# Kernel tuning notes

Hardware: AMD Instinct MI355X
Metric: run time of the kernel (lower is better)

Reference implementation:

```python
import jax, jax.numpy as jnp
import numpy as np
import math

N_HEADS = 12
ROPE_DIM = 64
BASE = 10000.0


def _rope_tables(seq_len, dim):
    inv_freq = 1.0 / (BASE ** (jnp.arange(0, dim, 2, dtype=jnp.float32) / dim))
    t = jnp.arange(seq_len, dtype=jnp.float32)
    freqs = jnp.outer(t, inv_freq)                      # [S, dim/2]
    emb = jnp.concatenate([freqs, freqs], axis=-1)      # [S, dim]
    # broadcast shape [1, S, 1, dim]
    return jnp.cos(emb)[None, :, None, :], jnp.sin(emb)[None, :, None, :]


def _rotate_half(x):
    x1, x2 = jnp.split(x, 2, axis=-1)
    return jnp.concatenate([-x2, x1], axis=-1)


def setup_inputs() -> dict:
    key = jax.random.key(0)
    ks = jax.random.split(key, 9)
    B, S, E = 2, 2048, 768
    s = 1.0 / math.sqrt(E)
    return {
        "x": jax.random.normal(ks[0], (B, S, E), jnp.float32),
        "Wq": jax.random.normal(ks[1], (E, E), jnp.float32) * s,
        "bq": jax.random.normal(ks[2], (E,), jnp.float32) * 0.02,
        "Wk": jax.random.normal(ks[3], (E, E), jnp.float32) * s,
        "bk": jax.random.normal(ks[4], (E,), jnp.float32) * 0.02,
        "Wv": jax.random.normal(ks[5], (E, E), jnp.float32) * s,
        "bv": jax.random.normal(ks[6], (E,), jnp.float32) * 0.02,
        "Wp": jax.random.normal(ks[7], (E, E), jnp.float32) * s,
        "bp": jax.random.normal(ks[8], (E,), jnp.float32) * 0.02,
    }


def reference(x, Wq, bq, Wk, bk, Wv, bv, Wp, bp):
    B, S, E = x.shape
    H = N_HEADS
    D = E // H

    q = (x @ Wq + bq).reshape(B, S, H, D)
    k = (x @ Wk + bk).reshape(B, S, H, D)
    v = (x @ Wv + bv).reshape(B, S, H, D)

    # rotary on first ROPE_DIM dims (here ROPE_DIM == D, so full rotary)
    cos, sin = _rope_tables(S, ROPE_DIM)
    q_rot, q_pass = q[..., :ROPE_DIM], q[..., ROPE_DIM:]
    k_rot, k_pass = k[..., :ROPE_DIM], k[..., ROPE_DIM:]
    q_rot = q_rot * cos + _rotate_half(q_rot) * sin
    k_rot = k_rot * cos + _rotate_half(k_rot) * sin
    q = jnp.concatenate([q_rot, q_pass], axis=-1)
    k = jnp.concatenate([k_rot, k_pass], axis=-1)

    # scores [B, M, N, H]; mask before scaling (as in the torch code; -inf unchanged)
    att = jnp.einsum("bmhd,bnhd->bmnh", q, k)
    causal = jnp.tril(jnp.ones((S, S), dtype=bool))[None, :, :, None]
    att = jnp.where(causal, att, -jnp.inf)
    att = jax.nn.softmax(att / math.sqrt(D), axis=2)
    out = jnp.einsum("bmnh,bnhd->bmhd", att, v)

    return out.reshape(B, S, E) @ Wp + bp
```

## Files before the change

### kernel.cpp

```cpp
#include <hip/hip_runtime.h>
#include <stdint.h>

#define S_LEN 2048
#define EMB   768
#define NH    12
#define DH    64
#define M_TOT 4096
#define WELEM 589824
#define QELEM 3145728

typedef float  floatx4 __attribute__((ext_vector_type(4)));
typedef __bf16 bf16x8  __attribute__((ext_vector_type(8)));
typedef __bf16 bf16x4  __attribute__((ext_vector_type(4)));
typedef unsigned short ushortx4 __attribute__((ext_vector_type(4)));

__device__ __forceinline__ unsigned short f2bf(float f) {
    union { float f; unsigned u; } v; v.f = f;
    unsigned u = v.u;
    unsigned r = (u + 0x7FFFu + ((u >> 16) & 1u)) >> 16;
    return (unsigned short)r;
}

__device__ __forceinline__ void gl_lds16(const void* g, void* l) {
    __builtin_amdgcn_global_load_lds(
        (__attribute__((address_space(1))) const void*)g,
        (__attribute__((address_space(3))) void*)l, 16, 0, 0);
}

__global__ void cvt_all_kernel(const float* __restrict__ x, unsigned short* __restrict__ xb,
                               const float* __restrict__ W0, const float* __restrict__ W1,
                               const float* __restrict__ W2, const float* __restrict__ W3,
                               unsigned short* __restrict__ WT_all, float2* __restrict__ rope) {
    __shared__ float t[64][65];
    const int blk = blockIdx.x;
    if (blk < 3072) {
        int i = (blk * 256 + threadIdx.x) * 4;
        float4 v = *(const float4*)(x + i);
        ushortx4 r = { f2bf(v.x), f2bf(v.y), f2bf(v.z), f2bf(v.w) };
        *(ushortx4*)(xb + i) = r;
        return;
    }
    if (blk >= 3648) {
        int idx = (blk - 3648) * 256 + threadIdx.x;
        int s = idx >> 5, d = idx & 31;
        float f = exp2f((float)d * -0.41524101186092034f);
        float th = (float)s * f;
        float sn, cs; sincosf(th, &sn, &cs);
        rope[idx] = make_float2(cs, sn);
        return;
    }
    const int tc = blk - 3072;
    const int z = tc / 144, rr0 = tc % 144;
    const float* W = (z == 0) ? W0 : (z == 1 ? W1 : (z == 2 ? W2 : W3));
    unsigned short* O = WT_all + (size_t)z * WELEM;
    const int k0 = (rr0 % 12) * 64, n0 = (rr0 / 12) * 64;
    const int c = threadIdx.x & 63, r4 = threadIdx.x >> 6;
#pragma unroll
    for (int rr = 0; rr < 64; rr += 4) {
        int r = rr + r4;
        t[r][c] = W[(size_t)(k0 + r) * EMB + n0 + c];
    }
    __syncthreads();
#pragma unroll
    for (int rr = 0; rr < 64; rr += 4) {
        int nn = rr + r4;
        O[(size_t)(n0 + nn) * EMB + k0 + c] = f2bf(t[c][nn]);
    }
}

static __device__ __forceinline__ void gemm_core_128x128(
    const unsigned short* __restrict__ A, const unsigned short* __restrict__ BT,
    int m0, int n0, int K, int tid, floatx4 (&acc)[4][4],
    unsigned short* Als, unsigned short* Bls)
{
    const int lane = tid & 63;
    const int c0 = lane & 15, quad = lane >> 4;
    const int wave = tid >> 6;
    const int wm = (wave >> 1) * 64, wn = (wave & 1) * 64;

    for (int k0 = 0; k0 < K; k0 += 64) {
        __syncthreads();
#pragma unroll
        for (int it = 0; it < 4; ++it) {
            int ch = it * 256 + tid;
            int row = ch >> 3, sc = ch & 7;
            int cc = sc ^ (row & 7);
            gl_lds16(A  + (size_t)(m0 + row) * K + k0 + cc * 8, Als + ch * 8);
            gl_lds16(BT + (size_t)(n0 + row) * K + k0 + cc * 8, Bls + ch * 8);
        }
        __syncthreads();
        bf16x8 af[4][2], bfv[4][2];
#pragma unroll
        for (int ii = 0; ii < 4; ++ii) {
            int row = wm + 16 * ii + c0;
#pragma unroll
            for (int h = 0; h < 2; ++h)
                af[ii][h] = *(const bf16x8*)(Als + row * 64 + (((4 * h + quad) ^ (row & 7)) * 8));
        }
#pragma unroll
        for (int jj = 0; jj < 4; ++jj) {
            int row = wn + 16 * jj + c0;
#pragma unroll
            for (int h = 0; h < 2; ++h)
                bfv[jj][h] = *(const bf16x8*)(Bls + row * 64 + (((4 * h + quad) ^ (row & 7)) * 8));
        }
#pragma unroll
        for (int ii = 0; ii < 4; ++ii)
#pragma unroll
            for (int jj = 0; jj < 4; ++jj) {
                acc[ii][jj] = __builtin_amdgcn_mfma_f32_16x16x32_bf16(af[ii][0], bfv[jj][0], acc[ii][jj], 0, 0, 0);
                acc[ii][jj] = __builtin_amdgcn_mfma_f32_16x16x32_bf16(af[ii][1], bfv[jj][1], acc[ii][jj], 0, 0, 0);
            }
    }
}

__global__ __launch_bounds__(256, 3) void qkv_kernel(
    const unsigned short* __restrict__ xb, const unsigned short* __restrict__ WT_all,
    const float* __restrict__ bq, const float* __restrict__ bk, const float* __restrict__ bv,
    const float2* __restrict__ rope, unsigned short* __restrict__ qkv_out)
{
    __shared__ __align__(16) unsigned short Als[128 * 64];
    __shared__ __align__(16) unsigned short Bls[128 * 64];
    const int z = blockIdx.z;
    const float* bias = (z == 0) ? bq : (z == 1 ? bk : bv);
    __bf16* Cout = (__bf16*)(qkv_out + (size_t)z * QELEM);
    const int m0 = blockIdx.x * 128, n0 = blockIdx.y * 128;
    const int tid = threadIdx.x, lane = tid & 63, c0 = lane & 15, quad = lane >> 4, wave = tid >> 6;
    const int wm = (wave >> 1) * 64, wn = (wave & 1) * 64;

    floatx4 acc[4][4] = {};
    gemm_core_128x128(xb, WT_all + (size_t)z * WELEM, m0, n0, EMB, tid, acc, Als, Bls);

    if (z == 2) {
#pragma unroll
        for (int ii = 0; ii < 4; ++ii) {
            int m = m0 + wm + 16 * ii + quad * 4;
            int b = m >> 11, s = m & (S_LEN - 1);
#pragma unroll
            for (int jj = 0; jj < 4; ++jj) {
                int n = n0 + wn + 16 * jj + c0;
                int h = n >> 6, d = n & 63;
                float bn = bias[n];
                bf16x4 pv;
#pragma unroll
                for (int r = 0; r < 4; ++r) pv[r] = (__bf16)(acc[ii][jj][r] + bn);
                *(bf16x4*)(Cout + ((size_t)(b * NH + h) * DH + d) * S_LEN + s) = pv;
            }
        }
        return;
    }

#pragma unroll
    for (int ii = 0; ii < 4; ++ii) {
#pragma unroll
        for (int r = 0; r < 4; ++r) {
            int m = m0 + wm + 16 * ii + quad * 4 + r;
            int b = m >> 11, s = m & (S_LEN - 1);
            float vals[4];
#pragma unroll
            for (int jj = 0; jj < 4; ++jj) vals[jj] = acc[ii][jj][r] + bias[n0 + wn + 16 * jj + c0];
#pragma unroll
            for (int jj = 0; jj < 2; ++jj) {
                int d = 16 * jj + c0;
                float2 t = rope[s * 32 + d];
                float lo = vals[jj], hi = vals[jj + 2];
                vals[jj]     = lo * t.x - hi * t.y;
                vals[jj + 2] = hi * t.x + lo * t.y;
            }
            if (z == 0) {
#pragma unroll
                for (int jj = 0; jj < 4; ++jj) vals[jj] *= 0.18033688011112042f;
            }
#pragma unroll
            for (int jj = 0; jj < 4; ++jj) {
                int n = n0 + wn + 16 * jj + c0;
                int h = n >> 6, d = n & 63;
                Cout[((size_t)(b * NH + h) * S_LEN + s) * DH + d] = (__bf16)vals[jj];
            }
        }
    }
}

__global__ __launch_bounds__(256, 2) void flash_kernel(
    const unsigned short* __restrict__ Qg, const unsigned short* __restrict__ Kg,
    const unsigned short* __restrict__ Vt, unsigned short* __restrict__ Og)
{
    __shared__ __align__(16) unsigned short Kls[3][64 * 64];
    __shared__ __align__(16) unsigned short Vls[3][64 * 64];
    __shared__ __align__(16) unsigned short Pls[4][16 * 72];

    const int i = blockIdx.x;
    const int kk = i >> 8, g = i & 255;
    const int r0 = (kk == 0) ? g : (kk == 1 ? 511 - g : 512 + g);
    const int qt = 31 - r0 / 24;
    const int bh = r0 % 24;
    const int b = bh / NH, h = bh % NH;
    const int m0 = qt * 64;
    const int tid = threadIdx.x, lane = tid & 63, wave = tid >> 6;
    const int c0 = lane & 15, quad = lane >> 4;
    const size_t base = (size_t)bh * S_LEN * DH;
    const int mrow = m0 + wave * 16 + c0;

    bf16x8 qf0 = *(const bf16x8*)(Qg + base + (size_t)mrow * DH + quad * 8);
    bf16x8 qf1 = *(const bf16x8*)(Qg + base + (size_t)mrow * DH + 32 + quad * 8);
    asm volatile("" :: "v"(qf0), "v"(qf1));

    floatx4 oa[4] = {};
    float l_lane = 0.f;
    const float C = 23.083120654223414f;
    const int ntiles = qt + 1;

#define STAGE_TILE(T, BUF)                                                              \
    {                                                                                   \
        _Pragma("unroll")                                                               \
        for (int it = 0; it < 2; ++it) {                                                \
            int ch = it * 256 + tid;                                                    \
            int row = ch >> 3, cc = (ch & 7) ^ (row & 7);                               \
            gl_lds16(Kg + base + (size_t)((T) * 64 + row) * DH + cc * 8,                \
                     &Kls[BUF][ch * 8]);                                                \
            gl_lds16(Vt + base + (size_t)row * S_LEN + (T) * 64 + cc * 8,               \
                     &Vls[BUF][ch * 8]);                                                \
        }                                                                               \
    }

    STAGE_TILE(0, 0);
    if (ntiles > 1) STAGE_TILE(1, 1);

    for (int nt = 0; nt < ntiles; ++nt) {
        const int buf = nt % 3;
        if (nt + 1 < ntiles) asm volatile("s_waitcnt vmcnt(4)" ::: "memory");
        else                 asm volatile("s_waitcnt vmcnt(0)" ::: "memory");
        __builtin_amdgcn_s_barrier();
        asm volatile("" ::: "memory");
        if (nt + 2 < ntiles) {
            STAGE_TILE(nt + 2, (nt + 2) % 3);
        }
        const unsigned short* Kb = Kls[buf];
        const unsigned short* Vb = Vls[buf];

        floatx4 sa[4];
        const floatx4 zz = { 0.f, 0.f, 0.f, 0.f };
        __builtin_amdgcn_s_setprio(1);
#pragma unroll
        for (int jj = 0; jj < 4; ++jj) {
            int row = 16 * jj + c0;
            bf16x8 k0 = *(const bf16x8*)(Kb + row * 64 + ((quad ^ (row & 7)) * 8));
            bf16x8 k1 = *(const bf16x8*)(Kb + row * 64 + (((4 + quad) ^ (row & 7)) * 8));
            sa[jj] = __builtin_amdgcn_mfma_f32_16x16x32_bf16(k0, qf0, zz, 0, 0, 0);
            sa[jj] = __builtin_amdgcn_mfma_f32_16x16x32_bf16(k1, qf1, sa[jj], 0, 0, 0);
        }
        __builtin_amdgcn_s_setprio(0);
        if (nt == ntiles - 1) {
#pragma unroll
            for (int jj = 0; jj < 4; ++jj) {
                int nb = m0 + 16 * jj + quad * 4;
#pragma unroll
                for (int rr = 0; rr < 4; ++rr)
                    if (nb + rr > mrow) sa[jj][rr] = -1e30f;
            }
        }
#pragma unroll
        for (int jj = 0; jj < 4; ++jj) {
            bf16x4 pw;
#pragma unroll
            for (int rr = 0; rr < 4; ++rr) {
                float p = __builtin_amdgcn_exp2f(sa[jj][rr] - C);
                l_lane += p;
                pw[rr] = (__bf16)p;
            }
            *(bf16x4*)(&Pls[wave][c0 * 72 + 16 * jj + quad * 4]) = pw;
        }
        __builtin_amdgcn_s_setprio(1);
#pragma unroll
        for (int h2 = 0; h2 < 2; ++h2) {
            bf16x8 pf = *(const bf16x8*)(&Pls[wave][c0 * 72 + 32 * h2 + quad * 8]);
#pragma unroll
            for (int dt = 0; dt < 4; ++dt) {
                int row = 16 * dt + c0;
                bf16x8 vf = *(const bf16x8*)(Vb + row * 64 + (((4 * h2 + quad) ^ (row & 7)) * 8));
                oa[dt] = __builtin_amdgcn_mfma_f32_16x16x32_bf16(vf, pf, oa[dt], 0, 0, 0);
            }
        }
        __builtin_amdgcn_s_setprio(0);
    }
#undef STAGE_TILE

    l_lane += __shfl_xor(l_lane, 16, 64);
    l_lane += __shfl_xor(l_lane, 32, 64);
    const float rl = 1.0f / l_lane;
    __bf16* Ob16 = (__bf16*)Og;
#pragma unroll
    for (int dt = 0; dt < 4; ++dt) {
        bf16x4 ov;
#pragma unroll
        for (int rr = 0; rr < 4; ++rr) ov[rr] = (__bf16)(oa[dt][rr] * rl);
        *(bf16x4*)(Ob16 + ((size_t)(b * S_LEN + mrow)) * EMB + h * DH + dt * 16 + quad * 4) = ov;
    }
}

__global__ __launch_bounds__(256, 3) void proj_kernel(
    const unsigned short* __restrict__ Ob, const unsigned short* __restrict__ WpT,
    const float* __restrict__ bp, float* __restrict__ out)
{
    __shared__ __align__(16) unsigned short Als[128 * 64];
    __shared__ __align__(16) unsigned short Bls[128 * 64];
    const int m0 = blockIdx.x * 128, n0 = blockIdx.y * 128;
    const int tid = threadIdx.x, lane = tid & 63, c0 = lane & 15, quad = lane >> 4, wave = tid >> 6;
    const int wm = (wave >> 1) * 64, wn = (wave & 1) * 64;

    floatx4 acc[4][4] = {};
    gemm_core_128x128(Ob, WpT, m0, n0, EMB, tid, acc, Als, Bls);

#pragma unroll
    for (int ii = 0; ii < 4; ++ii)
#pragma unroll
        for (int r = 0; r < 4; ++r) {
            int m = m0 + wm + 16 * ii + quad * 4 + r;
#pragma unroll
            for (int jj = 0; jj < 4; ++jj) {
                int n = n0 + wn + 16 * jj + c0;
                out[(size_t)m * EMB + n] = acc[ii][jj][r] + bp[n];
            }
        }
}

extern "C" void kernel_launch(void* const* d_in, const int* in_sizes, int n_in,
                              void* d_out, int out_size, void* d_ws, size_t ws_size,
                              hipStream_t stream)
{
    (void)in_sizes; (void)n_in; (void)out_size;
    const float* x  = (const float*)d_in[0];
    const float* Wq = (const float*)d_in[1];
    const float* bq = (const float*)d_in[2];
    const float* Wk = (const float*)d_in[3];
    const float* bk = (const float*)d_in[4];
    const float* Wv = (const float*)d_in[5];
    const float* bv = (const float*)d_in[6];
    const float* Wp = (const float*)d_in[7];
    const float* bp = (const float*)d_in[8];

    unsigned short* ws  = (unsigned short*)d_ws;
    unsigned short* xb  = ws;
    unsigned short* WT  = xb + (size_t)QELEM;
    unsigned short* QKV = WT + 4 * (size_t)WELEM;
    unsigned short* Ob  = QKV + 3 * (size_t)QELEM;
    float2* rope = (float2*)(Ob + (size_t)QELEM);
    if (ws_size < ((size_t)QELEM * 5 + 4 * (size_t)WELEM) * 2 + 2048 * 32 * 8) return;

    cvt_all_kernel<<<3904, 256, 0, stream>>>(x, xb, Wq, Wk, Wv, Wp, WT, rope);
    qkv_kernel<<<dim3(32, 6, 3), 256, 0, stream>>>(xb, WT, bq, bk, bv, (const float2*)rope, QKV);
    flash_kernel<<<dim3(768), 256, 0, stream>>>(QKV, QKV + QELEM, QKV + 2 * (size_t)QELEM, Ob);
    proj_kernel<<<dim3(32, 6), 256, 0, stream>>>(Ob, WT + 3 * (size_t)WELEM, bp, (float*)d_out);
}
```

Measured before the change: 156.1 us.

## Process 128 query rows per flash block to reuse K/V tiles

Each flash-attention block now covers 128 query rows instead of 64, with each wave computing two 16-row query fragments against the same staged K/V tile. This halves the number of blocks and the K/V tile loads and barriers per query row. The block-to-query mapping is reordered, and the causal mask is applied on the final two tiles. The trade-off is fewer blocks (384) to fill the GPU and load-balance the triangular work, plus higher register and LDS use per block.

Result: slower. 164.1 us (+5.2%).

```diff
diff --git a/kernel.cpp b/kernel.cpp
--- a/kernel.cpp
+++ b/kernel.cpp
@@ -187,28 +187,29 @@
 {
     __shared__ __align__(16) unsigned short Kls[3][64 * 64];
     __shared__ __align__(16) unsigned short Vls[3][64 * 64];
-    __shared__ __align__(16) unsigned short Pls[4][16 * 72];
+    __shared__ __align__(16) unsigned short Pls[8][16 * 72];
 
     const int i = blockIdx.x;
-    const int kk = i >> 8, g = i & 255;
-    const int r0 = (kk == 0) ? g : (kk == 1 ? 511 - g : 512 + g);
-    const int qt = 31 - r0 / 24;
-    const int bh = r0 % 24;
+    const int qblk = (i < 192) ? (i / 24) : (15 - (i - 192) / 24);
+    const int bh = i % 24;
     const int b = bh / NH, h = bh % NH;
-    const int m0 = qt * 64;
+    const int m0 = qblk * 128;
     const int tid = threadIdx.x, lane = tid & 63, wave = tid >> 6;
     const int c0 = lane & 15, quad = lane >> 4;
     const size_t base = (size_t)bh * S_LEN * DH;
-    const int mrow = m0 + wave * 16 + c0;
-
-    bf16x8 qf0 = *(const bf16x8*)(Qg + base + (size_t)mrow * DH + quad * 8);
-    bf16x8 qf1 = *(const bf16x8*)(Qg + base + (size_t)mrow * DH + 32 + quad * 8);
-    asm volatile("" :: "v"(qf0), "v"(qf1));
-
-    floatx4 oa[4] = {};
-    float l_lane = 0.f;
+    const int mrow0 = m0 + wave * 32 + c0;
+    const int mrow1 = mrow0 + 16;
+
+    bf16x8 qa0 = *(const bf16x8*)(Qg + base + (size_t)mrow0 * DH + quad * 8);
+    bf16x8 qa1 = *(const bf16x8*)(Qg + base + (size_t)mrow0 * DH + 32 + quad * 8);
+    bf16x8 qb0 = *(const bf16x8*)(Qg + base + (size_t)mrow1 * DH + quad * 8);
+    bf16x8 qb1 = *(const bf16x8*)(Qg + base + (size_t)mrow1 * DH + 32 + quad * 8);
+    asm volatile("" :: "v"(qa0), "v"(qa1), "v"(qb0), "v"(qb1));
+
+    floatx4 oa0[4] = {}, oa1[4] = {};
+    float l0 = 0.f, l1 = 0.f;
     const float C = 23.083120654223414f;
-    const int ntiles = qt + 1;
+    const int ntiles = 2 * qblk + 2;
 
 #define STAGE_TILE(T, BUF)                                                              \
     {                                                                                   \
@@ -224,7 +225,7 @@
     }
 
     STAGE_TILE(0, 0);
-    if (ntiles > 1) STAGE_TILE(1, 1);
+    STAGE_TILE(1, 1);
 
     for (int nt = 0; nt < ntiles; ++nt) {
         const int buf = nt % 3;
@@ -238,7 +239,7 @@
         const unsigned short* Kb = Kls[buf];
         const unsigned short* Vb = Vls[buf];
 
-        floatx4 sa[4];
+        floatx4 sa0[4], sa1[4];
         const floatx4 zz = { 0.f, 0.f, 0.f, 0.f };
         __builtin_amdgcn_s_setprio(1);
 #pragma unroll
@@ -246,55 +247,71 @@
             int row = 16 * jj + c0;
             bf16x8 k0 = *(const bf16x8*)(Kb + row * 64 + ((quad ^ (row & 7)) * 8));
             bf16x8 k1 = *(const bf16x8*)(Kb + row * 64 + (((4 + quad) ^ (row & 7)) * 8));
-            sa[jj] = __builtin_amdgcn_mfma_f32_16x16x32_bf16(k0, qf0, zz, 0, 0, 0);
-            sa[jj] = __builtin_amdgcn_mfma_f32_16x16x32_bf16(k1, qf1, sa[jj], 0, 0, 0);
+            sa0[jj] = __builtin_amdgcn_mfma_f32_16x16x32_bf16(k0, qa0, zz, 0, 0, 0);
+            sa0[jj] = __builtin_amdgcn_mfma_f32_16x16x32_bf16(k1, qa1, sa0[jj], 0, 0, 0);
+            sa1[jj] = __builtin_amdgcn_mfma_f32_16x16x32_bf16(k0, qb0, zz, 0, 0, 0);
+            sa1[jj] = __builtin_amdgcn_mfma_f32_16x16x32_bf16(k1, qb1, sa1[jj], 0, 0, 0);
         }
         __builtin_amdgcn_s_setprio(0);
-        if (nt == ntiles - 1) {
-#pragma unroll
-            for (int jj = 0; jj < 4; ++jj) {
-                int nb = m0 + 16 * jj + quad * 4;
-#pragma unroll
-                for (int rr = 0; rr < 4; ++rr)
-                    if (nb + rr > mrow) sa[jj][rr] = -1e30f;
+        if (nt >= ntiles - 2) {
+#pragma unroll
+            for (int jj = 0; jj < 4; ++jj) {
+                int nb = nt * 64 + 16 * jj + quad * 4;
+#pragma unroll
+                for (int rr = 0; rr < 4; ++rr) {
+                    if (nb + rr > mrow0) sa0[jj][rr] = -1e30f;
+                    if (nb + rr > mrow1) sa1[jj][rr] = -1e30f;
+                }
             }
         }
 #pragma unroll
         for (int jj = 0; jj < 4; ++jj) {
-            bf16x4 pw;
+            bf16x4 pw0, pw1;
 #pragma unroll
             for (int rr = 0; rr < 4; ++rr) {
-                float p = __builtin_amdgcn_exp2f(sa[jj][rr] - C);
-                l_lane += p;
-                pw[rr] = (__bf16)p;
-            }
-            *(bf16x4*)(&Pls[wave][c0 * 72 + 16 * jj + quad * 4]) = pw;
+                float p0 = __builtin_amdgcn_exp2f(sa0[jj][rr] - C);
+                float p1 = __builtin_amdgcn_exp2f(sa1[jj][rr] - C);
+                l0 += p0; l1 += p1;
+                pw0[rr] = (__bf16)p0;
+                pw1[rr] = (__bf16)p1;
+            }
+            *(bf16x4*)(&Pls[wave * 2 + 0][c0 * 72 + 16 * jj + quad * 4]) = pw0;
+            *(bf16x4*)(&Pls[wave * 2 + 1][c0 * 72 + 16 * jj + quad * 4]) = pw1;
         }
         __builtin_amdgcn_s_setprio(1);
 #pragma unroll
         for (int h2 = 0; h2 < 2; ++h2) {
-            bf16x8 pf = *(const bf16x8*)(&Pls[wave][c0 * 72 + 32 * h2 + quad * 8]);
+            bf16x8 pf0 = *(const bf16x8*)(&Pls[wave * 2 + 0][c0 * 72 + 32 * h2 + quad * 8]);
+            bf16x8 pf1 = *(const bf16x8*)(&Pls[wave * 2 + 1][c0 * 72 + 32 * h2 + quad * 8]);
 #pragma unroll
             for (int dt = 0; dt < 4; ++dt) {
                 int row = 16 * dt + c0;
                 bf16x8 vf = *(const bf16x8*)(Vb + row * 64 + (((4 * h2 + quad) ^ (row & 7)) * 8));
-                oa[dt] = __builtin_amdgcn_mfma_f32_16x16x32_bf16(vf, pf, oa[dt], 0, 0, 0);
+                oa0[dt] = __builtin_amdgcn_mfma_f32_16x16x32_bf16(vf, pf0, oa0[dt], 0, 0, 0);
+                oa1[dt] = __builtin_amdgcn_mfma_f32_16x16x32_bf16(vf, pf1, oa1[dt], 0, 0, 0);
             }
         }
         __builtin_amdgcn_s_setprio(0);
     }
 #undef STAGE_TILE
 
-    l_lane += __shfl_xor(l_lane, 16, 64);
-    l_lane += __shfl_xor(l_lane, 32, 64);
-    const float rl = 1.0f / l_lane;
+    l0 += __shfl_xor(l0, 16, 64);
+    l0 += __shfl_xor(l0, 32, 64);
+    l1 += __shfl_xor(l1, 16, 64);
+    l1 += __shfl_xor(l1, 32, 64);
+    const float rl0 = 1.0f / l0;
+    const float rl1 = 1.0f / l1;
     __bf16* Ob16 = (__bf16*)Og;
 #pragma unroll
     for (int dt = 0; dt < 4; ++dt) {
-        bf16x4 ov;
-#pragma unroll
-        for (int rr = 0; rr < 4; ++rr) ov[rr] = (__bf16)(oa[dt][rr] * rl);
-        *(bf16x4*)(Ob16 + ((size_t)(b * S_LEN + mrow)) * EMB + h * DH + dt * 16 + quad * 4) = ov;
+        bf16x4 ov0, ov1;
+#pragma unroll
+        for (int rr = 0; rr < 4; ++rr) {
+            ov0[rr] = (__bf16)(oa0[dt][rr] * rl0);
+            ov1[rr] = (__bf16)(oa1[dt][rr] * rl1);
+        }
+        *(bf16x4*)(Ob16 + ((size_t)(b * S_LEN + mrow0)) * EMB + h * DH + dt * 16 + quad * 4) = ov0;
+        *(bf16x4*)(Ob16 + ((size_t)(b * S_LEN + mrow1)) * EMB + h * DH + dt * 16 + quad * 4) = ov1;
     }
 }
 
@@ -349,6 +366,6 @@
 
     cvt_all_kernel<<<3904, 256, 0, stream>>>(x, xb, Wq, Wk, Wv, Wp, WT, rope);
     qkv_kernel<<<dim3(32, 6, 3), 256, 0, stream>>>(xb, WT, bq, bk, bv, (const float2*)rope, QKV);
-    flash_kernel<<<dim3(768), 256, 0, stream>>>(QKV, QKV + QELEM, QKV + 2 * (size_t)QELEM, Ob);
+    flash_kernel<<<dim3(384), 256, 0, stream>>>(QKV, QKV + QELEM, QKV + 2 * (size_t)QELEM, Ob);
     proj_kernel<<<dim3(32, 6), 256, 0, stream>>>(Ob, WT + 3 * (size_t)WELEM, bp, (float*)d_out);
 }
```

## Switch flash attention to 32x32x16 MFMA with 2x2 wave split and register P

Applied to the files above, without the earlier changes.

Restructures the flash kernel so four waves form a 2x2 grid over query rows and key columns. Each wave now uses 32x32x16 MFMAs for both QK^T and PV. The P tile is repacked through cross-lane shuffles instead of an LDS round trip, and the partial outputs and row sums of the two key halves are combined through shared memory at the end. Occupancy is raised to 3 blocks per CU. The intent is fewer MFMA issues, no P LDS traffic, and better latency hiding, at the cost of a final reduction step and possible register pressure under the tighter launch bound.

Result: no change. 156.1 us (+0.0%).

```diff
diff --git a/kernel.cpp b/kernel.cpp
--- a/kernel.cpp
+++ b/kernel.cpp
@@ -9,7 +9,8 @@
 #define WELEM 589824
 #define QELEM 3145728
 
-typedef float  floatx4 __attribute__((ext_vector_type(4)));
+typedef float  floatx4  __attribute__((ext_vector_type(4)));
+typedef float  floatx16 __attribute__((ext_vector_type(16)));
 typedef __bf16 bf16x8  __attribute__((ext_vector_type(8)));
 typedef __bf16 bf16x4  __attribute__((ext_vector_type(4)));
 typedef unsigned short ushortx4 __attribute__((ext_vector_type(4)));
@@ -181,13 +182,13 @@
     }
 }
 
-__global__ __launch_bounds__(256, 2) void flash_kernel(
+__global__ __launch_bounds__(256, 3) void flash_kernel(
     const unsigned short* __restrict__ Qg, const unsigned short* __restrict__ Kg,
     const unsigned short* __restrict__ Vt, unsigned short* __restrict__ Og)
 {
     __shared__ __align__(16) unsigned short Kls[3][64 * 64];
     __shared__ __align__(16) unsigned short Vls[3][64 * 64];
-    __shared__ __align__(16) unsigned short Pls[4][16 * 72];
+    __shared__ float lred[2][64];
 
     const int i = blockIdx.x;
     const int kk = i >> 8, g = i & 255;
@@ -197,15 +198,18 @@
     const int b = bh / NH, h = bh % NH;
     const int m0 = qt * 64;
     const int tid = threadIdx.x, lane = tid & 63, wave = tid >> 6;
-    const int c0 = lane & 15, quad = lane >> 4;
+    const int wm2 = wave >> 1, wn2 = wave & 1;
+    const int lr = lane & 31, hf = lane >> 5;
     const size_t base = (size_t)bh * S_LEN * DH;
-    const int mrow = m0 + wave * 16 + c0;
-
-    bf16x8 qf0 = *(const bf16x8*)(Qg + base + (size_t)mrow * DH + quad * 8);
-    bf16x8 qf1 = *(const bf16x8*)(Qg + base + (size_t)mrow * DH + 32 + quad * 8);
-    asm volatile("" :: "v"(qf0), "v"(qf1));
-
-    floatx4 oa[4] = {};
+    const int mrow = m0 + wm2 * 32 + lr;
+
+    bf16x8 qf[4];
+#pragma unroll
+    for (int t = 0; t < 4; ++t)
+        qf[t] = *(const bf16x8*)(Qg + base + (size_t)mrow * DH + 16 * t + 8 * hf);
+    asm volatile("" :: "v"(qf[0]), "v"(qf[1]), "v"(qf[2]), "v"(qf[3]));
+
+    floatx16 oa0 = {}, oa1 = {};
     float l_lane = 0.f;
     const float C = 23.083120654223414f;
     const int ntiles = qt + 1;
@@ -232,69 +236,101 @@
         else                 asm volatile("s_waitcnt vmcnt(0)" ::: "memory");
         __builtin_amdgcn_s_barrier();
         asm volatile("" ::: "memory");
-        if (nt + 2 < ntiles) {
-            STAGE_TILE(nt + 2, (nt + 2) % 3);
-        }
+        if (nt + 2 < ntiles) STAGE_TILE(nt + 2, (nt + 2) % 3);
         const unsigned short* Kb = Kls[buf];
         const unsigned short* Vb = Vls[buf];
 
-        floatx4 sa[4];
-        const floatx4 zz = { 0.f, 0.f, 0.f, 0.f };
+        floatx16 sa = {};
         __builtin_amdgcn_s_setprio(1);
 #pragma unroll
-        for (int jj = 0; jj < 4; ++jj) {
-            int row = 16 * jj + c0;
-            bf16x8 k0 = *(const bf16x8*)(Kb + row * 64 + ((quad ^ (row & 7)) * 8));
-            bf16x8 k1 = *(const bf16x8*)(Kb + row * 64 + (((4 + quad) ^ (row & 7)) * 8));
-            sa[jj] = __builtin_amdgcn_mfma_f32_16x16x32_bf16(k0, qf0, zz, 0, 0, 0);
-            sa[jj] = __builtin_amdgcn_mfma_f32_16x16x32_bf16(k1, qf1, sa[jj], 0, 0, 0);
+        for (int t = 0; t < 4; ++t) {
+            int row = wn2 * 32 + lr;
+            int ck = (2 * t + hf) ^ (row & 7);
+            bf16x8 kf = *(const bf16x8*)(Kb + row * 64 + ck * 8);
+            sa = __builtin_amdgcn_mfma_f32_32x32x16_bf16(kf, qf[t], sa, 0, 0, 0);
         }
         __builtin_amdgcn_s_setprio(0);
+
         if (nt == ntiles - 1) {
 #pragma unroll
-            for (int jj = 0; jj < 4; ++jj) {
-                int nb = m0 + 16 * jj + quad * 4;
-#pragma unroll
-                for (int rr = 0; rr < 4; ++rr)
-                    if (nb + rr > mrow) sa[jj][rr] = -1e30f;
-            }
-        }
-#pragma unroll
-        for (int jj = 0; jj < 4; ++jj) {
-            bf16x4 pw;
-#pragma unroll
-            for (int rr = 0; rr < 4; ++rr) {
-                float p = __builtin_amdgcn_exp2f(sa[jj][rr] - C);
-                l_lane += p;
-                pw[rr] = (__bf16)p;
-            }
-            *(bf16x4*)(&Pls[wave][c0 * 72 + 16 * jj + quad * 4]) = pw;
-        }
+            for (int r = 0; r < 16; ++r) {
+                int n = nt * 64 + wn2 * 32 + (r & 3) + 8 * (r >> 2) + 4 * hf;
+                if (n > mrow) sa[r] = -1e30f;
+            }
+        }
+
+        unsigned W[8];
+#pragma unroll
+        for (int q = 0; q < 8; ++q) {
+            float p0 = __builtin_amdgcn_exp2f(sa[2 * q] - C);
+            float p1 = __builtin_amdgcn_exp2f(sa[2 * q + 1] - C);
+            l_lane += p0 + p1;
+            union { __bf16 bb[2]; unsigned u; } w;
+            w.bb[0] = (__bf16)p0; w.bb[1] = (__bf16)p1;
+            W[q] = w.u;
+        }
+        bf16x8 pb[2];
+#pragma unroll
+        for (int t2 = 0; t2 < 2; ++t2) {
+            unsigned own0 = hf ? W[4 * t2 + 2] : W[4 * t2 + 0];
+            unsigned own1 = hf ? W[4 * t2 + 3] : W[4 * t2 + 1];
+            unsigned giv0 = hf ? W[4 * t2 + 0] : W[4 * t2 + 2];
+            unsigned giv1 = hf ? W[4 * t2 + 1] : W[4 * t2 + 3];
+            unsigned s0 = (unsigned)__shfl_xor((int)giv0, 32, 64);
+            unsigned s1 = (unsigned)__shfl_xor((int)giv1, 32, 64);
+            union { unsigned u[4]; bf16x8 v; } pk;
+            pk.u[0] = hf ? s0 : own0;
+            pk.u[1] = hf ? s1 : own1;
+            pk.u[2] = hf ? own0 : s0;
+            pk.u[3] = hf ? own1 : s1;
+            pb[t2] = pk.v;
+        }
+
         __builtin_amdgcn_s_setprio(1);
 #pragma unroll
-        for (int h2 = 0; h2 < 2; ++h2) {
-            bf16x8 pf = *(const bf16x8*)(&Pls[wave][c0 * 72 + 32 * h2 + quad * 8]);
-#pragma unroll
-            for (int dt = 0; dt < 4; ++dt) {
-                int row = 16 * dt + c0;
-                bf16x8 vf = *(const bf16x8*)(Vb + row * 64 + (((4 * h2 + quad) ^ (row & 7)) * 8));
-                oa[dt] = __builtin_amdgcn_mfma_f32_16x16x32_bf16(vf, pf, oa[dt], 0, 0, 0);
+        for (int dt = 0; dt < 2; ++dt) {
+            int d = 32 * dt + lr;
+#pragma unroll
+            for (int t2 = 0; t2 < 2; ++t2) {
+                int cv = (wn2 * 4 + 2 * t2 + hf) ^ (d & 7);
+                bf16x8 vf = *(const bf16x8*)(Vb + d * 64 + cv * 8);
+                if (dt == 0) oa0 = __builtin_amdgcn_mfma_f32_32x32x16_bf16(vf, pb[t2], oa0, 0, 0, 0);
+                else         oa1 = __builtin_amdgcn_mfma_f32_32x32x16_bf16(vf, pb[t2], oa1, 0, 0, 0);
             }
         }
         __builtin_amdgcn_s_setprio(0);
     }
 #undef STAGE_TILE
 
-    l_lane += __shfl_xor(l_lane, 16, 64);
     l_lane += __shfl_xor(l_lane, 32, 64);
-    const float rl = 1.0f / l_lane;
-    __bf16* Ob16 = (__bf16*)Og;
-#pragma unroll
-    for (int dt = 0; dt < 4; ++dt) {
-        bf16x4 ov;
-#pragma unroll
-        for (int rr = 0; rr < 4; ++rr) ov[rr] = (__bf16)(oa[dt][rr] * rl);
-        *(bf16x4*)(Ob16 + ((size_t)(b * S_LEN + mrow)) * EMB + h * DH + dt * 16 + quad * 4) = ov;
+
+    __syncthreads();
+    float* red = (float*)&Kls[0][0];
+    if (wn2 == 1) {
+#pragma unroll
+        for (int e = 0; e < 16; ++e) red[(wm2 * 32 + e) * 64 + lane]        = oa0[e];
+#pragma unroll
+        for (int e = 0; e < 16; ++e) red[(wm2 * 32 + 16 + e) * 64 + lane]   = oa1[e];
+        lred[wm2][lane] = l_lane;
+    }
+    __syncthreads();
+    if (wn2 == 0) {
+        const float lt = l_lane + lred[wm2][lane];
+        const float rl = 1.0f / lt;
+        __bf16* Ob16 = (__bf16*)Og;
+#pragma unroll
+        for (int rg = 0; rg < 4; ++rg) {
+            bf16x4 ov0, ov1;
+#pragma unroll
+            for (int j = 0; j < 4; ++j) {
+                int e = rg * 4 + j;
+                ov0[j] = (__bf16)((oa0[e] + red[(wm2 * 32 + e) * 64 + lane]) * rl);
+                ov1[j] = (__bf16)((oa1[e] + red[(wm2 * 32 + 16 + e) * 64 + lane]) * rl);
+            }
+            int d = 8 * rg + 4 * hf;
+            *(bf16x4*)(Ob16 + ((size_t)(b * S_LEN + mrow)) * EMB + h * DH + d)      = ov0;
+            *(bf16x4*)(Ob16 + ((size_t)(b * S_LEN + mrow)) * EMB + h * DH + 32 + d) = ov1;
+        }
     }
 }
 
```
